# Optimization experiments

Measured on AMD Instinct MI355X. Metric: run time of the kernel, lower is better.

Reference implementation:

```python
import jax, jax.numpy as jnp
import numpy as np

N_NODES = 50000
N_EDGES = 1_000_000
D = 256


def gcn_conv(x, src, dst, ew, W, b, n):
    # PyG GCNConv with edge_weight: linear transform, add self-loops (w=1),
    # symmetric normalization deg^{-1/2} w deg^{-1/2}, scatter-sum, + bias.
    x = x @ W  # (n, out)
    loop = jnp.arange(n)
    src_l = jnp.concatenate([src, loop])
    dst_l = jnp.concatenate([dst, loop])
    ew_l = jnp.concatenate([ew, jnp.ones((n,), ew.dtype)])
    deg = jax.ops.segment_sum(ew_l, dst_l, num_segments=n)
    dinv = jnp.where(deg > 0, jax.lax.rsqrt(deg), 0.0).astype(x.dtype)
    norm = dinv[src_l] * ew_l * dinv[dst_l]  # (E+n,)
    out = jax.ops.segment_sum(norm[:, None] * x[src_l], dst_l, num_segments=n)
    return out + b


def setup_inputs() -> dict:
    key = jax.random.key(0)
    k = jax.random.split(key, 8)
    glorot = 1.0 / np.sqrt(D)
    return {
        "x": jax.random.normal(k[0], (N_NODES, D), jnp.float32),
        "edge_index": jax.random.randint(k[1], (2, N_EDGES), 0, N_NODES, jnp.int64),
        "edge_weight": jax.random.uniform(k[2], (N_EDGES,), jnp.float32),
        "W1": jax.random.normal(k[3], (D, D), jnp.float32) * glorot,
        "b1": jnp.zeros((D,), jnp.float32),
        "W2": jax.random.normal(k[4], (D, D), jnp.float32) * glorot,
        "b2": jnp.zeros((D,), jnp.float32),
    }


def reference(x, edge_index, edge_weight, W1, b1, W2, b2):
    n = x.shape[0]
    src, dst = edge_index[0], edge_index[1]
    h = gcn_conv(x, src, dst, edge_weight, W1, b1, n)
    h = jax.nn.relu(h)  # dropout is identity at eval
    out = gcn_conv(h, src, dst, edge_weight, W2, b2, n)
    return out
```

## Files before the change

### kernel.cpp

```cpp
#include <hip/hip_runtime.h>
#include <hip/hip_bf16.h>
#include <stdint.h>


#define D 256
#define CAP 64

typedef __attribute__((ext_vector_type(8))) short short8;
typedef __attribute__((ext_vector_type(4))) float floatx4;

__device__ inline unsigned short f2bf_rne(float f) {
    union { float f; uint32_t u; } v; v.f = f;
    uint32_t u = v.u;
    return (unsigned short)((u + 0x7FFFu + ((u >> 16) & 1u)) >> 16);
}
__device__ inline float bf_lo(uint32_t u) { union { uint32_t u; float f; } v; v.u = u << 16; return v.f; }
__device__ inline float bf_hi(uint32_t u) { union { uint32_t u; float f; } v; v.u = u & 0xFFFF0000u; return v.f; }

#define FXS 16777216.0f

#define GBM 128
#define GBN 128
#define GBK 32
#define LDA 40
#define NB_CVT 64
#define NB_P1 1600

__device__ void gemm1_block(const float* __restrict__ x, const float* __restrict__ W1,
                            unsigned short* __restrict__ C, int n, int bid,
                            unsigned char* smem) {
    unsigned short (*As)[LDA] = (unsigned short(*)[LDA])smem;
    unsigned short (*Bs)[LDA] = (unsigned short(*)[LDA])(smem + GBM * LDA * 2);
    int t = threadIdx.x;
    int bm = (bid >> 1) * GBM;
    int bn = (bid & 1) * GBN;
    int w = t >> 6, l = t & 63;
    int wm = (w >> 1) * 64, wn = (w & 1) * 64;
    int lr = l & 15;
    int lq = l >> 4;
    floatx4 acc[4][4] = {};
    for (int k0 = 0; k0 < D; k0 += GBK) {
        #pragma unroll
        for (int i = 0; i < 2; i++) {
            int c = t + i * 256;
            int row = c >> 2;
            int kk = (c & 3) * 8;
            int gr = bm + row;
            short8 av = {};
            if (gr < n) {
                const float* ap = x + (size_t)gr * D + k0 + kk;
                float4 f0 = *(const float4*)ap;
                float4 f1 = *(const float4*)(ap + 4);
                av[0] = (short)f2bf_rne(f0.x); av[1] = (short)f2bf_rne(f0.y);
                av[2] = (short)f2bf_rne(f0.z); av[3] = (short)f2bf_rne(f0.w);
                av[4] = (short)f2bf_rne(f1.x); av[5] = (short)f2bf_rne(f1.y);
                av[6] = (short)f2bf_rne(f1.z); av[7] = (short)f2bf_rne(f1.w);
            }
            *(short8*)&As[row][kk] = av;
        }
        #pragma unroll
        for (int i = 0; i < 4; i++) {
            int idx = t + i * 256;
            int kk = idx >> 5;
            int nn4 = (idx & 31) << 2;
            float4 wv = *(const float4*)(W1 + (size_t)(k0 + kk) * D + bn + nn4);
            Bs[nn4 + 0][kk] = f2bf_rne(wv.x);
            Bs[nn4 + 1][kk] = f2bf_rne(wv.y);
            Bs[nn4 + 2][kk] = f2bf_rne(wv.z);
            Bs[nn4 + 3][kk] = f2bf_rne(wv.w);
        }
        __syncthreads();
        short8 af[4], bfr[4];
        #pragma unroll
        for (int i = 0; i < 4; i++) af[i] = *(const short8*)&As[wm + i * 16 + lr][lq * 8];
        #pragma unroll
        for (int j = 0; j < 4; j++) bfr[j] = *(const short8*)&Bs[wn + j * 16 + lr][lq * 8];
        #pragma unroll
        for (int i = 0; i < 4; i++)
            #pragma unroll
            for (int j = 0; j < 4; j++)
                acc[i][j] = __builtin_amdgcn_mfma_f32_16x16x32_bf16(af[i], bfr[j], acc[i][j], 0, 0, 0);
        __syncthreads();
    }
    #pragma unroll
    for (int i = 0; i < 4; i++) {
        #pragma unroll
        for (int r = 0; r < 4; r++) {
            int row = bm + wm + i * 16 + lq * 4 + r;
            if (row >= n) continue;
            #pragma unroll
            for (int j = 0; j < 4; j++) {
                int col = bn + wn + j * 16 + lr;
                C[(size_t)row * D + col] = f2bf_rne(acc[i][j][r]);
            }
        }
    }
}

__device__ void cvtw2_block(const float* __restrict__ W2, unsigned short* __restrict__ Wt,
                            int bid, unsigned char* smem) {
    float (*sw)[33] = (float(*)[33])smem;
    int k0 = (bid >> 3) * 32, n0 = (bid & 7) * 32;
    int t = threadIdx.x;
    int tx = t & 31, ty0 = (t >> 5) * 4;
    #pragma unroll
    for (int r = 0; r < 4; r++)
        sw[ty0 + r][tx] = W2[(size_t)(k0 + ty0 + r) * D + n0 + tx];
    __syncthreads();
    #pragma unroll
    for (int r = 0; r < 4; r++)
        Wt[(size_t)(n0 + ty0 + r) * D + k0 + tx] = f2bf_rne(sw[tx][ty0 + r]);
}

__device__ void pass1_block(const int* __restrict__ src, const int* __restrict__ dst,
                            const float* __restrict__ ew,
                            unsigned long long* __restrict__ packed,
                            unsigned long long* __restrict__ edata, int E, int bid, int nb) {
    int stride = nb * 256;
    for (int e = bid * 256 + threadIdx.x; e < E; e += stride) {
        int d = __builtin_nontemporal_load(&dst[e]);
        float w = __builtin_nontemporal_load(&ew[e]);
        uint32_t fx = __float2uint_rn(w * FXS);
        unsigned long long old =
            atomicAdd(&packed[(size_t)d << 3], ((unsigned long long)fx << 32) | 1ull);
        uint32_t r = (uint32_t)old;
        if (r < CAP) {
            int s = __builtin_nontemporal_load(&src[e]);
            unsigned long long pv =
                ((unsigned long long)__float_as_uint(w) << 32) | (uint32_t)s;
            edata[((size_t)d << 6) + r] = pv;
        }
    }
}

__global__ __launch_bounds__(256) void fused1_kernel(const float* __restrict__ x,
                                                     const float* __restrict__ W1,
                                                     const float* __restrict__ W2,
                                                     const int* __restrict__ src,
                                                     const int* __restrict__ dst,
                                                     const float* __restrict__ ew,
                                                     unsigned short* __restrict__ xws,
                                                     unsigned short* __restrict__ w2t,
                                                     unsigned long long* __restrict__ packed,
                                                     unsigned long long* __restrict__ edata,
                                                     int n, int E, int nb_gemm) {
    __shared__ unsigned char smem[2 * GBM * LDA * 2];
    int bid = blockIdx.x;
    if (bid < nb_gemm) {
        gemm1_block(x, W1, xws, n, bid, smem);
    } else if (bid < nb_gemm + NB_CVT) {
        cvtw2_block(W2, w2t, bid - nb_gemm, smem);
    } else {
        pass1_block(src, dst, ew, packed, edata, E, bid - nb_gemm - NB_CVT, NB_P1);
    }
}

__global__ void unpack_kernel(const unsigned long long* __restrict__ packed,
                              float* __restrict__ dinv, int n) {
    int i = blockIdx.x * 256 + threadIdx.x;
    if (i < n) {
        float deg = (float)(packed[(size_t)i << 3] >> 32) * (1.0f / FXS) + 1.0f;
        dinv[i] = rsqrtf(deg);
    }
}

__global__ __launch_bounds__(256) void gemm2_kernel(const unsigned short* __restrict__ A,
                                                    const unsigned short* __restrict__ Bt,
                                                    unsigned short* __restrict__ C, int n) {
    __shared__ unsigned short As[GBM][LDA];
    __shared__ unsigned short Bs[GBN][LDA];
    int t = threadIdx.x;
    int bm = blockIdx.x * GBM;
    int bn = blockIdx.y * GBN;
    int w = t >> 6, l = t & 63;
    int wm = (w >> 1) * 64, wn = (w & 1) * 64;
    int lr = l & 15;
    int lq = l >> 4;
    floatx4 acc[4][4] = {};
    for (int k0 = 0; k0 < D; k0 += GBK) {
        #pragma unroll
        for (int i = 0; i < 2; i++) {
            int c = t + i * 256;
            int row = c >> 2;
            int kk = (c & 3) * 8;
            int gr = bm + row;
            short8 av = {};
            if (gr < n) av = *(const short8*)&A[(size_t)gr * D + k0 + kk];
            *(short8*)&As[row][kk] = av;
            short8 bv = *(const short8*)&Bt[(size_t)(bn + row) * D + k0 + kk];
            *(short8*)&Bs[row][kk] = bv;
        }
        __syncthreads();
        short8 af[4], bfr[4];
        #pragma unroll
        for (int i = 0; i < 4; i++) af[i] = *(const short8*)&As[wm + i * 16 + lr][lq * 8];
        #pragma unroll
        for (int j = 0; j < 4; j++) bfr[j] = *(const short8*)&Bs[wn + j * 16 + lr][lq * 8];
        #pragma unroll
        for (int i = 0; i < 4; i++)
            #pragma unroll
            for (int j = 0; j < 4; j++)
                acc[i][j] = __builtin_amdgcn_mfma_f32_16x16x32_bf16(af[i], bfr[j], acc[i][j], 0, 0, 0);
        __syncthreads();
    }
    #pragma unroll
    for (int i = 0; i < 4; i++) {
        #pragma unroll
        for (int r = 0; r < 4; r++) {
            int row = bm + wm + i * 16 + lq * 4 + r;
            if (row >= n) continue;
            #pragma unroll
            for (int j = 0; j < 4; j++) {
                int col = bn + wn + j * 16 + lr;
                C[(size_t)row * D + col] = f2bf_rne(acc[i][j][r]);
            }
        }
    }
}

template <bool RELU, bool OUT_BF16>
__global__ __launch_bounds__(256) void gather_kernel(const unsigned short* __restrict__ xw,
                                                     const uint2* __restrict__ edata,
                                                     const unsigned long long* __restrict__ packed,
                                                     const float* __restrict__ dinv,
                                                     const float* __restrict__ bias,
                                                     void* __restrict__ outv, int n) {
    int wid = threadIdx.x >> 6;
    int lane = threadIdx.x & 63;
    int node = (blockIdx.x << 2) + wid;
    if (node >= n) return;
    int half = lane >> 5;
    int cl = lane & 31;
    int ch = cl << 3;
    float di = dinv[node];

    float acc[8];
    {
        uint4 r = *(const uint4*)(xw + (size_t)node * D + ch);
        float4 b0 = *(const float4*)(bias + ch);
        float4 b1 = *(const float4*)(bias + ch + 4);
        float ws = (half == 0) ? di * di : 0.0f;
        float bs = (half == 0) ? 1.0f : 0.0f;
        acc[0] = ws * bf_lo(r.x) + bs * b0.x;
        acc[1] = ws * bf_hi(r.x) + bs * b0.y;
        acc[2] = ws * bf_lo(r.y) + bs * b0.z;
        acc[3] = ws * bf_hi(r.y) + bs * b0.w;
        acc[4] = ws * bf_lo(r.z) + bs * b1.x;
        acc[5] = ws * bf_hi(r.z) + bs * b1.y;
        acc[6] = ws * bf_lo(r.w) + bs * b1.z;
        acc[7] = ws * bf_hi(r.w) + bs * b1.w;
    }

    int cnt = (int)(uint32_t)packed[(size_t)node << 3];
    cnt = min(cnt, CAP);
    const uint2* ebase = edata + ((size_t)node << 6);

    for (int j = 0; j < cnt; j += 8) {
        #pragma unroll
        for (int k = 0; k < 4; k++) {
            int e = j + 2 * k + half;
            bool valid = e < cnt;
            uint2 m; m.x = (uint32_t)node; m.y = 0u;
            if (valid) m = ebase[e];
            float co = dinv[m.x] * __uint_as_float(m.y) * di;
            uint4 r = *(const uint4*)(xw + (size_t)m.x * D + ch);
            acc[0] += co * bf_lo(r.x);
            acc[1] += co * bf_hi(r.x);
            acc[2] += co * bf_lo(r.y);
            acc[3] += co * bf_hi(r.y);
            acc[4] += co * bf_lo(r.z);
            acc[5] += co * bf_hi(r.z);
            acc[6] += co * bf_lo(r.w);
            acc[7] += co * bf_hi(r.w);
        }
    }
    #pragma unroll
    for (int k = 0; k < 8; k++) acc[k] += __shfl_xor(acc[k], 32);

    if (RELU) {
        #pragma unroll
        for (int k = 0; k < 8; k++) acc[k] = fmaxf(acc[k], 0.0f);
    }
    if (OUT_BF16) {
        if (half == 0) {
            uint4 o;
            o.x = (uint32_t)f2bf_rne(acc[0]) | ((uint32_t)f2bf_rne(acc[1]) << 16);
            o.y = (uint32_t)f2bf_rne(acc[2]) | ((uint32_t)f2bf_rne(acc[3]) << 16);
            o.z = (uint32_t)f2bf_rne(acc[4]) | ((uint32_t)f2bf_rne(acc[5]) << 16);
            o.w = (uint32_t)f2bf_rne(acc[6]) | ((uint32_t)f2bf_rne(acc[7]) << 16);
            *(uint4*)((unsigned short*)outv + (size_t)node * D + ch) = o;
        }
    } else {
        floatx4 o;
        int b = half * 4;
        o[0] = acc[b + 0]; o[1] = acc[b + 1]; o[2] = acc[b + 2]; o[3] = acc[b + 3];
        __builtin_nontemporal_store(o, (floatx4*)((float*)outv + (size_t)node * D + ch + b));
    }
}

extern "C" void kernel_launch(void* const* d_in, const int* in_sizes, int n_in,
                              void* d_out, int out_size, void* d_ws, size_t ws_size,
                              hipStream_t stream) {
    const float* x  = (const float*)d_in[0];
    const int*   ei = (const int*)d_in[1];
    const float* ew = (const float*)d_in[2];
    const float* W1 = (const float*)d_in[3];
    const float* b1 = (const float*)d_in[4];
    const float* W2 = (const float*)d_in[5];
    const float* b2 = (const float*)d_in[6];
    float* out = (float*)d_out;

    const int n = in_sizes[0] / D;
    const int E = in_sizes[2];
    const int* src = ei;
    const int* dst = ei + E;

    char* ws = (char*)d_ws;
    size_t off = 0;
    auto carve = [&](size_t bytes) {
        char* p = ws + off;
        off = (off + bytes + 255) & ~(size_t)255;
        return p;
    };
    unsigned long long* packed = (unsigned long long*)carve((size_t)n * 64);
    float*          dinv = (float*)carve((size_t)n * 4);
    unsigned long long* edata = (unsigned long long*)carve((size_t)n * CAP * 8);
    unsigned short* w2t  = (unsigned short*)carve((size_t)D * D * 2);
    unsigned short* xws  = (unsigned short*)carve((size_t)n * D * 2);
    unsigned short* hb   = (unsigned short*)carve((size_t)n * D * 2);

    const int nb_gemm = ((n + GBM - 1) / GBM) * 2;
    const int nb_node = (n + 255) / 256;

    (void)hipMemsetAsync(packed, 0, (size_t)n * 64, stream);

    fused1_kernel<<<nb_gemm + NB_CVT + NB_P1, 256, 0, stream>>>(
        x, W1, W2, src, dst, ew, xws, w2t, packed, edata, n, E, nb_gemm);

    unpack_kernel<<<nb_node, 256, 0, stream>>>(packed, dinv, n);

    dim3 agrid((n + 3) / 4);
    gather_kernel<true, true><<<agrid, 256, 0, stream>>>(xws, (const uint2*)edata, packed, dinv, b1, hb, n);

    dim3 ggrid((n + GBM - 1) / GBM, D / GBN);
    gemm2_kernel<<<ggrid, 256, 0, stream>>>(hb, w2t, xws, n);

    gather_kernel<false, false><<<agrid, 256, 0, stream>>>(xws, (const uint2*)edata, packed, dinv, b2, out, n);
}
```

Measured before the change: 362.8 us.

## Precompute edge coefficients once and gather with half-wave per node

Adds a coef_kernel that folds dinv[src]*w*dinv[dst] into the edge data once, so both gather passes read a ready coefficient instead of doing a dependent dinv lookup per edge. The gather kernel now gives each node 32 lanes instead of 64. Eight edge records are loaded cooperatively and broadcast with shuffles, which removes the cross-half reduction and the idle half on stores. The cost is an extra kernel launch and a read-modify-write over the edge array, and each lane now processes edges serially with more loads in flight per lane.

Measured after the change: 372.1 us. 2.6% more time.

```diff
diff --git a/kernel.cpp b/kernel.cpp
--- a/kernel.cpp
+++ b/kernel.cpp
@@ -164,6 +164,22 @@
     }
 }
 
+__global__ __launch_bounds__(256) void coef_kernel(const unsigned long long* __restrict__ packed,
+                                                   uint2* __restrict__ edata,
+                                                   const float* __restrict__ dinv, int n) {
+    int node = blockIdx.x * 4 + (threadIdx.x >> 6);
+    if (node >= n) return;
+    int l = threadIdx.x & 63;
+    int cnt = min((int)(uint32_t)packed[(size_t)node << 3], CAP);
+    float dd = dinv[node];
+    if (l < cnt) {
+        uint2 v = edata[((size_t)node << 6) + l];
+        float co = dinv[v.x] * __uint_as_float(v.y) * dd;
+        v.y = __float_as_uint(co);
+        edata[((size_t)node << 6) + l] = v;
+    }
+}
+
 __global__ __launch_bounds__(256) void gemm2_kernel(const unsigned short* __restrict__ A,
                                                     const unsigned short* __restrict__ Bt,
                                                     unsigned short* __restrict__ C, int n) {
@@ -225,12 +241,10 @@
                                                      const float* __restrict__ dinv,
                                                      const float* __restrict__ bias,
                                                      void* __restrict__ outv, int n) {
-    int wid = threadIdx.x >> 6;
-    int lane = threadIdx.x & 63;
-    int node = (blockIdx.x << 2) + wid;
+    int g = threadIdx.x >> 5;
+    int cl = threadIdx.x & 31;
+    int node = (blockIdx.x << 3) + g;
     if (node >= n) return;
-    int half = lane >> 5;
-    int cl = lane & 31;
     int ch = cl << 3;
     float di = dinv[node];
 
@@ -239,31 +253,30 @@
         uint4 r = *(const uint4*)(xw + (size_t)node * D + ch);
         float4 b0 = *(const float4*)(bias + ch);
         float4 b1 = *(const float4*)(bias + ch + 4);
-        float ws = (half == 0) ? di * di : 0.0f;
-        float bs = (half == 0) ? 1.0f : 0.0f;
-        acc[0] = ws * bf_lo(r.x) + bs * b0.x;
-        acc[1] = ws * bf_hi(r.x) + bs * b0.y;
-        acc[2] = ws * bf_lo(r.y) + bs * b0.z;
-        acc[3] = ws * bf_hi(r.y) + bs * b0.w;
-        acc[4] = ws * bf_lo(r.z) + bs * b1.x;
-        acc[5] = ws * bf_hi(r.z) + bs * b1.y;
-        acc[6] = ws * bf_lo(r.w) + bs * b1.z;
-        acc[7] = ws * bf_hi(r.w) + bs * b1.w;
-    }
-
-    int cnt = (int)(uint32_t)packed[(size_t)node << 3];
-    cnt = min(cnt, CAP);
+        float ws = di * di;
+        acc[0] = ws * bf_lo(r.x) + b0.x;
+        acc[1] = ws * bf_hi(r.x) + b0.y;
+        acc[2] = ws * bf_lo(r.y) + b0.z;
+        acc[3] = ws * bf_hi(r.y) + b0.w;
+        acc[4] = ws * bf_lo(r.z) + b1.x;
+        acc[5] = ws * bf_hi(r.z) + b1.y;
+        acc[6] = ws * bf_lo(r.w) + b1.z;
+        acc[7] = ws * bf_hi(r.w) + b1.w;
+    }
+
+    int cnt = min((int)(uint32_t)packed[(size_t)node << 3], CAP);
     const uint2* ebase = edata + ((size_t)node << 6);
 
     for (int j = 0; j < cnt; j += 8) {
-        #pragma unroll
-        for (int k = 0; k < 4; k++) {
-            int e = j + 2 * k + half;
-            bool valid = e < cnt;
-            uint2 m; m.x = (uint32_t)node; m.y = 0u;
-            if (valid) m = ebase[e];
-            float co = dinv[m.x] * __uint_as_float(m.y) * di;
-            uint4 r = *(const uint4*)(xw + (size_t)m.x * D + ch);
+        uint2 md; md.x = (uint32_t)node; md.y = 0u;
+        if (cl < 8 && j + cl < cnt) md = ebase[j + cl];
+        int mx = (int)md.x;
+        int my = (int)md.y;
+        #pragma unroll
+        for (int k = 0; k < 8; k++) {
+            int srck = __shfl(mx, k, 32);
+            float co = __uint_as_float((uint32_t)__shfl(my, k, 32));
+            uint4 r = *(const uint4*)(xw + (size_t)srck * D + ch);
             acc[0] += co * bf_lo(r.x);
             acc[1] += co * bf_hi(r.x);
             acc[2] += co * bf_lo(r.y);
@@ -274,27 +287,25 @@
             acc[7] += co * bf_hi(r.w);
         }
     }
-    #pragma unroll
-    for (int k = 0; k < 8; k++) acc[k] += __shfl_xor(acc[k], 32);
 
     if (RELU) {
         #pragma unroll
         for (int k = 0; k < 8; k++) acc[k] = fmaxf(acc[k], 0.0f);
     }
     if (OUT_BF16) {
-        if (half == 0) {
-            uint4 o;
-            o.x = (uint32_t)f2bf_rne(acc[0]) | ((uint32_t)f2bf_rne(acc[1]) << 16);
-            o.y = (uint32_t)f2bf_rne(acc[2]) | ((uint32_t)f2bf_rne(acc[3]) << 16);
-            o.z = (uint32_t)f2bf_rne(acc[4]) | ((uint32_t)f2bf_rne(acc[5]) << 16);
-            o.w = (uint32_t)f2bf_rne(acc[6]) | ((uint32_t)f2bf_rne(acc[7]) << 16);
-            *(uint4*)((unsigned short*)outv + (size_t)node * D + ch) = o;
-        }
+        uint4 o;
+        o.x = (uint32_t)f2bf_rne(acc[0]) | ((uint32_t)f2bf_rne(acc[1]) << 16);
+        o.y = (uint32_t)f2bf_rne(acc[2]) | ((uint32_t)f2bf_rne(acc[3]) << 16);
+        o.z = (uint32_t)f2bf_rne(acc[4]) | ((uint32_t)f2bf_rne(acc[5]) << 16);
+        o.w = (uint32_t)f2bf_rne(acc[6]) | ((uint32_t)f2bf_rne(acc[7]) << 16);
+        *(uint4*)((unsigned short*)outv + (size_t)node * D + ch) = o;
     } else {
-        floatx4 o;
-        int b = half * 4;
-        o[0] = acc[b + 0]; o[1] = acc[b + 1]; o[2] = acc[b + 2]; o[3] = acc[b + 3];
-        __builtin_nontemporal_store(o, (floatx4*)((float*)outv + (size_t)node * D + ch + b));
+        floatx4 o0, o1;
+        o0[0] = acc[0]; o0[1] = acc[1]; o0[2] = acc[2]; o0[3] = acc[3];
+        o1[0] = acc[4]; o1[1] = acc[5]; o1[2] = acc[6]; o1[3] = acc[7];
+        float* op = (float*)outv + (size_t)node * D + ch;
+        __builtin_nontemporal_store(o0, (floatx4*)op);
+        __builtin_nontemporal_store(o1, (floatx4*)(op + 4));
     }
 }
 
@@ -339,7 +350,9 @@
 
     unpack_kernel<<<nb_node, 256, 0, stream>>>(packed, dinv, n);
 
-    dim3 agrid((n + 3) / 4);
+    coef_kernel<<<(n + 3) / 4, 256, 0, stream>>>(packed, (uint2*)edata, dinv, n);
+
+    dim3 agrid((n + 7) / 8);
     gather_kernel<true, true><<<agrid, 256, 0, stream>>>(xws, (const uint2*)edata, packed, dinv, b1, hb, n);
 
     dim3 ggrid((n + GBM - 1) / GBM, D / GBN);
```
